# Performance work log

Hardware: AMD Instinct MI355X
Metric: run time of the kernel (lower is better)

Reference implementation:

```python
import jax, jax.numpy as jnp
import numpy as np

B, F, H, S, K, L, C = 128, 8192, 8192, 4, 32, 3, 100  # batch, encoded feats, hidden, segments, synapses/seg, hidden layers, classes


def setup_inputs() -> dict:
    key = jax.random.key(0)
    k1, k2, k3, k4, k5, k6 = jax.random.split(key, 6)
    # binary encoded input activations (thermometer-coded tabular features)
    x = jax.random.randint(k1, (B, F), 0, 2).astype(jnp.float32)
    # sign weights in {-1,+1} for each synapse of each segment of each neuron
    signs0 = jnp.where(jax.random.bernoulli(k2, 0.5, (S, H, K)), 1.0, -1.0).astype(jnp.float32)
    signsH = jnp.where(jax.random.bernoulli(k3, 0.5, (L - 1, S, H, K)), 1.0, -1.0).astype(jnp.float32)
    # synapse source indices (irregular connectivity)
    idx0 = jax.random.randint(k4, (S, H, K), 0, F, dtype=jnp.int32)
    idxH = jax.random.randint(k5, (L - 1, S, H, K), 0, H, dtype=jnp.int32)
    # per-layer output connection matrices [L, H, C]
    wout = jax.random.normal(k6, (L, H, C), dtype=jnp.float32) * 0.02
    return {"x": x, "signs0": signs0, "signsH": signsH, "wout": wout,
            "idx0": idx0, "idxH": idxH, "threshold": 8}


def _segment_layer(a, idx, signs, threshold):
    # a: [B, P] prev activations; idx/signs: [S, H, K]
    g = a[:, idx]                                  # [B, S, H, K] irregular gather
    z = jnp.einsum('bshk,shk->bsh', g, signs)      # per-segment summed input
    fired = jnp.any(z >= threshold, axis=1)        # OR over segments -> [B, H]
    return fired.astype(a.dtype)


def reference(x, signs0, signsH, wout, idx0, idxH, threshold):
    thr = jnp.float32(threshold)
    a = _segment_layer(x, idx0, signs0, thr)       # hidden layer 0
    acts = [a]
    for l in range(idxH.shape[0]):                 # remaining hidden layers (fixed small L)
        a = _segment_layer(a, idxH[l], signsH[l], thr)
        acts.append(a)
    # sum class votes from every hidden layer's output connection matrix
    out = jnp.einsum('lbh,lhc->bc', jnp.stack(acts, 0), wout)  # [B, C]
    return out
```

## Files before the change

### kernel.cpp

```cpp
#include <hip/hip_runtime.h>
#include <stdint.h>

#define B 128
#define F 8192
#define H 8192
#define S 4
#define K 32
#define L 3
#define C 100


__global__ void pack_x_kernel(const float* __restrict__ x, uint2* __restrict__ xPP,
                              float* __restrict__ out) {
    const int zi = blockIdx.x * 128 + threadIdx.x;
    if (zi < B * C) out[zi] = 0.0f;

    const int b  = threadIdx.x;
    const int wv = threadIdx.x >> 6;
    const int f0 = blockIdx.x * 32;
    const float4* xr = (const float4*)(x + (size_t)b * F + f0);
    for (int j = 0; j < 8; ++j) {
        const float4 v = xr[j];
        const uint64_t m0 = __ballot(v.x > 0.5f);
        const uint64_t m1 = __ballot(v.y > 0.5f);
        const uint64_t m2 = __ballot(v.z > 0.5f);
        const uint64_t m3 = __ballot(v.w > 0.5f);
        if ((threadIdx.x & 63) == 0) {
            const int f = f0 + 4 * j;
            uint4* dst = (uint4*)(xPP + (size_t)wv * F + f);
            dst[0] = make_uint4((uint32_t)m0, (uint32_t)(m0 >> 32),
                                (uint32_t)m1, (uint32_t)(m1 >> 32));
            dst[1] = make_uint4((uint32_t)m2, (uint32_t)(m2 >> 32),
                                (uint32_t)m3, (uint32_t)(m3 >> 32));
        }
    }
}

__device__ __forceinline__ int load_threshold(const int* p) {
    int v = *p;
    if (v >= (1 << 23)) v = (int)__int_as_float(v);
    return v;
}

__device__ __forceinline__ void cs5(uint32_t* a, uint32_t v) {
#pragma unroll
    for (int i = 0; i < 5; ++i) { const uint32_t t = a[i]; a[i] = t ^ v; v = t & v; }
}

__device__ __forceinline__ void pair_sum5(const uint32_t* x, uint32_t* y) {
    uint32_t c = 0;
#pragma unroll
    for (int i = 0; i < 5; ++i) {
        const uint32_t p = (uint32_t)__shfl_xor((int)x[i], 32);
        const uint32_t s = x[i] ^ p;
        y[i] = s ^ c;
        c = (x[i] & p) | (s & c);
    }
    y[5] = c;
}

__device__ __forceinline__ uint32_t fired_cmp(const uint32_t* A, const uint32_t* P, int thr) {
    uint32_t Y[7];
    uint32_t c = 0;
#pragma unroll
    for (int i = 0; i < 7; ++i) {
        const uint32_t ai = (i < 6) ? A[i] : 0u;
        const uint32_t bm = ((thr >> i) & 1) ? 0xFFFFFFFFu : 0u;
        const uint32_t t  = ai ^ bm;
        Y[i] = t ^ c;
        c = (ai & bm) | (t & c);
    }
    uint32_t bw = 0;
#pragma unroll
    for (int i = 0; i < 7; ++i) {
        const uint32_t xx = (i >= 1) ? P[i - 1] : 0u;
        const uint32_t d  = xx ^ Y[i];
        bw = ((~xx) & Y[i]) | ((~d) & bw);
    }
    return ~bw;
}

#define GLDS16(gp, lp)                                                \
    __builtin_amdgcn_global_load_lds(                                 \
        (const __attribute__((address_space(1))) uint32_t*)(gp),      \
        (__attribute__((address_space(3))) uint32_t*)(lp), 16, 0, 0)

#define HG 32
#define ISTRIDE 35

__global__ __launch_bounds__(512, 2) void layer_kernel(
        const uint32_t* __restrict__ prevPP,
        const int* __restrict__ idx,
        const float* __restrict__ signs,
        uint32_t* __restrict__ outPP,
        const int* __restrict__ thrp) {
    __shared__ uint2    tab[2 * H];
    __shared__ uint32_t isg[S * HG * ISTRIDE];
    __shared__ uint32_t fbuf[8 * HG * 2];

    const int tid = threadIdx.x;
    const int hg  = blockIdx.x;
    const int thr = load_threshold(thrp);

    {
        uint32_t* lbase = (uint32_t*)&tab[0];
#pragma unroll
        for (int i = 0; i < 16; ++i) {
            const int o = (i * 512 + tid) * 4;
            GLDS16(prevPP + o, lbase + o);
        }
    }
    {
        const int s    = tid >> 7;
        const int hrow = (tid & 127) >> 2;
        const int k0   = (tid & 3) * 8;
        const size_t gb = ((size_t)s * H + (size_t)hg * HG + hrow) * K + k0;
        const int4   ia = *(const int4*)(idx + gb);
        const int4   ic = *(const int4*)(idx + gb + 4);
        const float4 sa = *(const float4*)(signs + gb);
        const float4 sc = *(const float4*)(signs + gb + 4);
        uint32_t* dst = &isg[(s * HG + hrow) * ISTRIDE + k0];
        dst[0] = (uint32_t)ia.x | ((uint32_t)__float_as_int(sa.x) & 0x80000000u);
        dst[1] = (uint32_t)ia.y | ((uint32_t)__float_as_int(sa.y) & 0x80000000u);
        dst[2] = (uint32_t)ia.z | ((uint32_t)__float_as_int(sa.z) & 0x80000000u);
        dst[3] = (uint32_t)ia.w | ((uint32_t)__float_as_int(sa.w) & 0x80000000u);
        dst[4] = (uint32_t)ic.x | ((uint32_t)__float_as_int(sc.x) & 0x80000000u);
        dst[5] = (uint32_t)ic.y | ((uint32_t)__float_as_int(sc.y) & 0x80000000u);
        dst[6] = (uint32_t)ic.z | ((uint32_t)__float_as_int(sc.z) & 0x80000000u);
        dst[7] = (uint32_t)ic.w | ((uint32_t)__float_as_int(sc.w) & 0x80000000u);
    }
    __syncthreads();

    const int lane = tid & 63;
    const int ww   = tid >> 6;
    const int s    = ww & 3;
    const int wp   = ww >> 2;
    const int kh   = lane >> 5;
    const int h5   = lane & 31;

    uint32_t A0[5] = {0,0,0,0,0}, P0[5] = {0,0,0,0,0};
    uint32_t A1[5] = {0,0,0,0,0}, P1[5] = {0,0,0,0,0};
    const uint32_t* row = &isg[(s * HG + h5) * ISTRIDE + kh * 16];
    const uint2*    tw  = &tab[wp * H];
#pragma unroll
    for (int c8 = 0; c8 < 2; ++c8) {
        uint32_t iv[8];
#pragma unroll
        for (int j = 0; j < 8; ++j) iv[j] = row[c8 * 8 + j];
        uint2 g[8];
#pragma unroll
        for (int j = 0; j < 8; ++j) g[j] = tw[iv[j] & 0xFFFFu];
#pragma unroll
        for (int j = 0; j < 8; ++j) {
            const uint32_t pm = ~(uint32_t)((int32_t)iv[j] >> 31);
            cs5(A0, g[j].x);
            cs5(P0, g[j].x & pm);
            cs5(A1, g[j].y);
            cs5(P1, g[j].y & pm);
        }
    }

    uint32_t A0f[6], P0f[6], A1f[6], P1f[6];
    pair_sum5(A0, A0f);
    pair_sum5(P0, P0f);
    pair_sum5(A1, A1f);
    pair_sum5(P1, P1f);

    const uint32_t f0 = fired_cmp(A0f, P0f, thr);
    const uint32_t f1 = fired_cmp(A1f, P1f, thr);

    if (kh == 0) {
        fbuf[(ww * HG + h5) * 2 + 0] = f0;
        fbuf[(ww * HG + h5) * 2 + 1] = f1;
    }
    __syncthreads();

    if (tid < 128) {
        const int wp2  = tid >> 6;
        const int comp = (tid >> 5) & 1;
        const int hh   = tid & 31;
        uint32_t v = 0;
#pragma unroll
        for (int s2 = 0; s2 < 4; ++s2)
            v |= fbuf[((wp2 * 4 + s2) * HG + hh) * 2 + comp];
        outPP[((size_t)wp2 * H + (size_t)hg * HG + hh) * 2 + comp] = v;
    }
}

#define NHC 32
#define HCH (H / NHC)

__global__ void final_kernel(const uint32_t* __restrict__ actU,
                             const float* __restrict__ wout,
                             float* __restrict__ out) {
    const int lane = threadIdx.x & 63;
    const int wid  = threadIdx.x >> 6;
    const int hc   = blockIdx.x & (NHC - 1);
    const int bg   = blockIdx.x / NHC;
    const int b    = bg * 4 + wid;
    const int w32  = b >> 5;
    const int wp   = w32 >> 1;
    const int comp = w32 & 1;
    const int bit  = b & 31;

    float acc0 = 0.0f, acc1 = 0.0f;
    const int c1 = 64 + lane;
    const bool c1v = (c1 < C);

    for (int l = 0; l < L; ++l) {
        const uint32_t* aT = actU + ((size_t)(l * 2 + wp) * H) * 2 + comp;
        const float* wl = wout + (size_t)l * H * C;
        for (int r = 0; r < HCH / 64; ++r) {
            const int hbase = hc * HCH + r * 64;
            const uint32_t m = aT[(size_t)(hbase + lane) * 2];
            uint64_t hm = __ballot((m >> bit) & 1u);
            while (hm) {
                const int slot = __ffsll((unsigned long long)hm) - 1;
                hm &= hm - 1;
                const float* wr = wl + (size_t)(hbase + slot) * C;
                acc0 += wr[lane];
                if (c1v) acc1 += wr[c1];
            }
        }
    }
    atomicAdd(&out[b * C + lane], acc0);
    if (c1v) atomicAdd(&out[b * C + c1], acc1);
}

extern "C" void kernel_launch(void* const* d_in, const int* in_sizes, int n_in,
                              void* d_out, int out_size, void* d_ws, size_t ws_size,
                              hipStream_t stream) {
    const float* x      = (const float*)d_in[0];
    const float* signs0 = (const float*)d_in[1];
    const float* signsH = (const float*)d_in[2];
    const float* wout   = (const float*)d_in[3];
    const int*   idx0   = (const int*)d_in[4];
    const int*   idxH   = (const int*)d_in[5];
    const int*   thr    = (const int*)d_in[6];
    float* out = (float*)d_out;

    uint32_t* xPP   = (uint32_t*)d_ws;
    uint32_t* actPP = xPP + (size_t)4 * F;

    pack_x_kernel<<<F / 32, 128, 0, stream>>>(x, (uint2*)xPP, out);

    layer_kernel<<<H / HG, 512, 0, stream>>>(xPP, idx0, signs0, actPP, thr);
    layer_kernel<<<H / HG, 512, 0, stream>>>(actPP, idxH, signsH,
                                             actPP + (size_t)4 * H, thr);
    layer_kernel<<<H / HG, 512, 0, stream>>>(actPP + (size_t)4 * H,
                                             idxH + (size_t)S * H * K,
                                             signsH + (size_t)S * H * K,
                                             actPP + (size_t)8 * H, thr);

    final_kernel<<<32 * NHC, 256, 0, stream>>>(actPP, wout, out);
}
```

Before: 117.5 us.

## Fuse pack, three layers and readout into one cooperative kernel with grid syncs

Replaces the five separate launches (bit-pack, three layer kernels, final readout) with a single cooperative kernel of 256 blocks that uses grid-wide syncs between phases. The aim is to remove per-launch overhead and inter-kernel gaps, which matter because each phase is only tens of microseconds. In exchange it relies on all 256 blocks fitting co-resident, remaps the pack and final phases onto 512-thread blocks, and adds grid.sync costs. It falls back to the old multi-kernel path if the cooperative launch fails.

```diff
diff --git a/kernel.cpp b/kernel.cpp
--- a/kernel.cpp
+++ b/kernel.cpp
@@ -1,5 +1,8 @@
 #include <hip/hip_runtime.h>
+#include <hip/hip_cooperative_groups.h>
 #include <stdint.h>
+
+namespace cg = cooperative_groups;
 
 #define B 128
 #define F 8192
@@ -10,32 +13,6 @@
 #define C 100
 
 
-__global__ void pack_x_kernel(const float* __restrict__ x, uint2* __restrict__ xPP,
-                              float* __restrict__ out) {
-    const int zi = blockIdx.x * 128 + threadIdx.x;
-    if (zi < B * C) out[zi] = 0.0f;
-
-    const int b  = threadIdx.x;
-    const int wv = threadIdx.x >> 6;
-    const int f0 = blockIdx.x * 32;
-    const float4* xr = (const float4*)(x + (size_t)b * F + f0);
-    for (int j = 0; j < 8; ++j) {
-        const float4 v = xr[j];
-        const uint64_t m0 = __ballot(v.x > 0.5f);
-        const uint64_t m1 = __ballot(v.y > 0.5f);
-        const uint64_t m2 = __ballot(v.z > 0.5f);
-        const uint64_t m3 = __ballot(v.w > 0.5f);
-        if ((threadIdx.x & 63) == 0) {
-            const int f = f0 + 4 * j;
-            uint4* dst = (uint4*)(xPP + (size_t)wv * F + f);
-            dst[0] = make_uint4((uint32_t)m0, (uint32_t)(m0 >> 32),
-                                (uint32_t)m1, (uint32_t)(m1 >> 32));
-            dst[1] = make_uint4((uint32_t)m2, (uint32_t)(m2 >> 32),
-                                (uint32_t)m3, (uint32_t)(m3 >> 32));
-        }
-    }
-}
-
 __device__ __forceinline__ int load_threshold(const int* p) {
     int v = *p;
     if (v >= (1 << 23)) v = (int)__int_as_float(v);
@@ -88,22 +65,15 @@
 #define HG 32
 #define ISTRIDE 35
 
-__global__ __launch_bounds__(512, 2) void layer_kernel(
+__device__ __forceinline__ void layer_phase(
         const uint32_t* __restrict__ prevPP,
         const int* __restrict__ idx,
         const float* __restrict__ signs,
         uint32_t* __restrict__ outPP,
-        const int* __restrict__ thrp) {
-    __shared__ uint2    tab[2 * H];
-    __shared__ uint32_t isg[S * HG * ISTRIDE];
-    __shared__ uint32_t fbuf[8 * HG * 2];
-
-    const int tid = threadIdx.x;
-    const int hg  = blockIdx.x;
-    const int thr = load_threshold(thrp);
-
+        const int thr, const int hg, const int tid,
+        uint2* tab, uint32_t* isg, uint32_t* fbuf) {
     {
-        uint32_t* lbase = (uint32_t*)&tab[0];
+        uint32_t* lbase = (uint32_t*)tab;
 #pragma unroll
         for (int i = 0; i < 16; ++i) {
             const int o = (i * 512 + tid) * 4;
@@ -187,6 +157,140 @@
     }
 }
 
+__global__ __launch_bounds__(512, 2) void fused_kernel(
+        const float* __restrict__ x,
+        const int* __restrict__ idx0, const float* __restrict__ signs0,
+        const int* __restrict__ idxH, const float* __restrict__ signsH,
+        const float* __restrict__ wout, const int* __restrict__ thrp,
+        uint2* __restrict__ xPP, uint32_t* __restrict__ actPP,
+        float* __restrict__ out) {
+    __shared__ uint2    tab[2 * H];
+    __shared__ uint32_t isg[S * HG * ISTRIDE];
+    __shared__ uint32_t fbuf[8 * HG * 2];
+
+    cg::grid_group grid = cg::this_grid();
+    const int tid = threadIdx.x;
+    const int bid = blockIdx.x;
+    const int thr = load_threshold(thrp);
+
+    {
+        const int zi = bid * 512 + tid;
+        if (zi < B * C) out[zi] = 0.0f;
+
+        const int b   = tid & 127;
+        const int wv  = (tid >> 6) & 1;
+        const int sub = tid >> 7;
+        const int f0  = bid * 32;
+        const float4* xr = (const float4*)(x + (size_t)b * F + f0);
+#pragma unroll
+        for (int jj = 0; jj < 2; ++jj) {
+            const int j = sub * 2 + jj;
+            const float4 v = xr[j];
+            const uint64_t m0 = __ballot(v.x > 0.5f);
+            const uint64_t m1 = __ballot(v.y > 0.5f);
+            const uint64_t m2 = __ballot(v.z > 0.5f);
+            const uint64_t m3 = __ballot(v.w > 0.5f);
+            if ((tid & 63) == 0) {
+                const int f = f0 + 4 * j;
+                uint4* dst = (uint4*)(xPP + (size_t)wv * F + f);
+                dst[0] = make_uint4((uint32_t)m0, (uint32_t)(m0 >> 32),
+                                    (uint32_t)m1, (uint32_t)(m1 >> 32));
+                dst[1] = make_uint4((uint32_t)m2, (uint32_t)(m2 >> 32),
+                                    (uint32_t)m3, (uint32_t)(m3 >> 32));
+            }
+        }
+    }
+    __threadfence();
+    grid.sync();
+
+    layer_phase((const uint32_t*)xPP, idx0, signs0, actPP,
+                thr, bid, tid, tab, isg, fbuf);
+    __threadfence();
+    grid.sync();
+
+    layer_phase(actPP, idxH, signsH, actPP + (size_t)4 * H,
+                thr, bid, tid, tab, isg, fbuf);
+    __threadfence();
+    grid.sync();
+
+    layer_phase(actPP + (size_t)4 * H, idxH + (size_t)S * H * K,
+                signsH + (size_t)S * H * K, actPP + (size_t)8 * H,
+                thr, bid, tid, tab, isg, fbuf);
+    __threadfence();
+    grid.sync();
+
+    {
+        const int lane = tid & 63;
+        const int gw   = bid * 8 + (tid >> 6);
+        const int b    = gw >> 4;
+        const int hc   = gw & 15;
+        const int w32  = b >> 5;
+        const int wp   = w32 >> 1;
+        const int comp = w32 & 1;
+        const int bit  = b & 31;
+
+        float acc0 = 0.0f, acc1 = 0.0f;
+        const int c1 = 64 + lane;
+        const bool c1v = (c1 < C);
+
+        for (int l = 0; l < L; ++l) {
+            const uint32_t* aT = actPP + ((size_t)(l * 2 + wp) * H) * 2 + comp;
+            const float* wl = wout + (size_t)l * H * C;
+            for (int r = 0; r < 8; ++r) {
+                const int hbase = hc * 512 + r * 64;
+                const uint32_t m = aT[(size_t)(hbase + lane) * 2];
+                uint64_t hm = __ballot((m >> bit) & 1u);
+                while (hm) {
+                    const int slot = __ffsll((unsigned long long)hm) - 1;
+                    hm &= hm - 1;
+                    const float* wr = wl + (size_t)(hbase + slot) * C;
+                    acc0 += wr[lane];
+                    if (c1v) acc1 += wr[c1];
+                }
+            }
+        }
+        atomicAdd(&out[b * C + lane], acc0);
+        if (c1v) atomicAdd(&out[b * C + c1], acc1);
+    }
+}
+
+__global__ void pack_x_kernel(const float* __restrict__ x, uint2* __restrict__ xPP,
+                              float* __restrict__ out) {
+    const int zi = blockIdx.x * 128 + threadIdx.x;
+    if (zi < B * C) out[zi] = 0.0f;
+
+    const int b  = threadIdx.x;
+    const int wv = threadIdx.x >> 6;
+    const int f0 = blockIdx.x * 32;
+    const float4* xr = (const float4*)(x + (size_t)b * F + f0);
+    for (int j = 0; j < 8; ++j) {
+        const float4 v = xr[j];
+        const uint64_t m0 = __ballot(v.x > 0.5f);
+        const uint64_t m1 = __ballot(v.y > 0.5f);
+        const uint64_t m2 = __ballot(v.z > 0.5f);
+        const uint64_t m3 = __ballot(v.w > 0.5f);
+        if ((threadIdx.x & 63) == 0) {
+            const int f = f0 + 4 * j;
+            uint4* dst = (uint4*)(xPP + (size_t)wv * F + f);
+            dst[0] = make_uint4((uint32_t)m0, (uint32_t)(m0 >> 32),
+                                (uint32_t)m1, (uint32_t)(m1 >> 32));
+            dst[1] = make_uint4((uint32_t)m2, (uint32_t)(m2 >> 32),
+                                (uint32_t)m3, (uint32_t)(m3 >> 32));
+        }
+    }
+}
+
+__global__ __launch_bounds__(512, 2) void layer_kernel(
+        const uint32_t* __restrict__ prevPP, const int* __restrict__ idx,
+        const float* __restrict__ signs, uint32_t* __restrict__ outPP,
+        const int* __restrict__ thrp) {
+    __shared__ uint2    tab[2 * H];
+    __shared__ uint32_t isg[S * HG * ISTRIDE];
+    __shared__ uint32_t fbuf[8 * HG * 2];
+    layer_phase(prevPP, idx, signs, outPP, load_threshold(thrp),
+                blockIdx.x, threadIdx.x, tab, isg, fbuf);
+}
+
 #define NHC 32
 #define HCH (H / NHC)
 
@@ -241,16 +345,24 @@
 
     uint32_t* xPP   = (uint32_t*)d_ws;
     uint32_t* actPP = xPP + (size_t)4 * F;
-
-    pack_x_kernel<<<F / 32, 128, 0, stream>>>(x, (uint2*)xPP, out);
-
-    layer_kernel<<<H / HG, 512, 0, stream>>>(xPP, idx0, signs0, actPP, thr);
-    layer_kernel<<<H / HG, 512, 0, stream>>>(actPP, idxH, signsH,
-                                             actPP + (size_t)4 * H, thr);
-    layer_kernel<<<H / HG, 512, 0, stream>>>(actPP + (size_t)4 * H,
-                                             idxH + (size_t)S * H * K,
-                                             signsH + (size_t)S * H * K,
-                                             actPP + (size_t)8 * H, thr);
-
-    final_kernel<<<32 * NHC, 256, 0, stream>>>(actPP, wout, out);
-}
+    uint2*    xPP2  = (uint2*)d_ws;
+
+    void* args[] = { (void*)&x, (void*)&idx0, (void*)&signs0,
+                     (void*)&idxH, (void*)&signsH, (void*)&wout, (void*)&thr,
+                     (void*)&xPP2, (void*)&actPP, (void*)&out };
+    hipError_t e = hipLaunchCooperativeKernel((const void*)fused_kernel,
+                                              dim3(256), dim3(512),
+                                              args, 0, stream);
+    if (e != hipSuccess) {
+        (void)hipGetLastError();
+        pack_x_kernel<<<F / 32, 128, 0, stream>>>(x, xPP2, out);
+        layer_kernel<<<H / HG, 512, 0, stream>>>(xPP, idx0, signs0, actPP, thr);
+        layer_kernel<<<H / HG, 512, 0, stream>>>(actPP, idxH, signsH,
+                                                 actPP + (size_t)4 * H, thr);
+        layer_kernel<<<H / HG, 512, 0, stream>>>(actPP + (size_t)4 * H,
+                                                 idxH + (size_t)S * H * K,
+                                                 signsH + (size_t)S * H * K,
+                                                 actPP + (size_t)8 * H, thr);
+        final_kernel<<<32 * NHC, 256, 0, stream>>>(actPP, wout, out);
+    }
+}
```

Result: slower. 374.0 us (+218.3%).

## Fuse three layer kernels and final vote into one persistent kernel with grid barriers

Applied to the files above, without the earlier changes.

Replaces the three per-layer launches and the final vote kernel with one persistent kernel of 256 blocks. The batch is split into two 64-row halves, each handled by its own block group, so every block keeps only its half's activation table in LDS. Layers are separated by a software grid barrier per half, built from atomic counters that the pack kernel zeroes. The goal is to remove launch gaps and shrink LDS use to raise occupancy, at the cost of a spin barrier that assumes all blocks are co-resident and breaks out after a bounded wait.

```diff
diff --git a/kernel.cpp b/kernel.cpp
--- a/kernel.cpp
+++ b/kernel.cpp
@@ -9,11 +9,187 @@
 #define L 3
 #define C 100
 
-
-__global__ void pack_x_kernel(const float* __restrict__ x, uint2* __restrict__ xPP,
-                              float* __restrict__ out) {
+#define NBLK 256
+#define NTHR 512
+
+
+__device__ __forceinline__ int load_threshold(const int* p) {
+    int v = *p;
+    if (v >= (1 << 23)) v = (int)__int_as_float(v);
+    return v;
+}
+
+__device__ __forceinline__ void cs5(uint32_t* a, uint32_t v) {
+#pragma unroll
+    for (int i = 0; i < 5; ++i) { const uint32_t t = a[i]; a[i] = t ^ v; v = t & v; }
+}
+
+__device__ __forceinline__ void pair_sum5(const uint32_t* x, uint32_t* y) {
+    uint32_t c = 0;
+#pragma unroll
+    for (int i = 0; i < 5; ++i) {
+        const uint32_t p = (uint32_t)__shfl_xor((int)x[i], 32);
+        const uint32_t s = x[i] ^ p;
+        y[i] = s ^ c;
+        c = (x[i] & p) | (s & c);
+    }
+    y[5] = c;
+}
+
+__device__ __forceinline__ uint32_t fired_cmp(const uint32_t* A, const uint32_t* P, int thr) {
+    uint32_t Y[7];
+    uint32_t c = 0;
+#pragma unroll
+    for (int i = 0; i < 7; ++i) {
+        const uint32_t ai = (i < 6) ? A[i] : 0u;
+        const uint32_t bm = ((thr >> i) & 1) ? 0xFFFFFFFFu : 0u;
+        const uint32_t t  = ai ^ bm;
+        Y[i] = t ^ c;
+        c = (ai & bm) | (t & c);
+    }
+    uint32_t bw = 0;
+#pragma unroll
+    for (int i = 0; i < 7; ++i) {
+        const uint32_t xx = (i >= 1) ? P[i - 1] : 0u;
+        const uint32_t d  = xx ^ Y[i];
+        bw = ((~xx) & Y[i]) | ((~d) & bw);
+    }
+    return ~bw;
+}
+
+#define GLDS16(gp, lp)                                                \
+    __builtin_amdgcn_global_load_lds(                                 \
+        (const __attribute__((address_space(1))) uint32_t*)(gp),      \
+        (__attribute__((address_space(3))) uint32_t*)(lp), 16, 0, 0)
+
+#define AG_LOAD(p)                                                          \
+    __hip_atomic_load((p), __ATOMIC_RELAXED, __HIP_MEMORY_SCOPE_AGENT)
+#define AG_STORE(p, v)                                                      \
+    __hip_atomic_store((p), (v), __ATOMIC_RELAXED, __HIP_MEMORY_SCOPE_AGENT)
+
+__device__ __forceinline__ void wp_barrier(uint32_t* wbar, uint32_t ep,
+                                           int tid, int gidx) {
+    asm volatile("s_waitcnt vmcnt(0)" ::: "memory");
+    __syncthreads();
+    if (tid == 0) {
+        const uint32_t t = __hip_atomic_fetch_add(&wbar[gidx * 16], 1u,
+                               __ATOMIC_RELAXED, __HIP_MEMORY_SCOPE_AGENT) + 1u;
+        if (t == ep * 16u) {
+            const uint32_t r = __hip_atomic_fetch_add(&wbar[128], 1u,
+                               __ATOMIC_RELAXED, __HIP_MEMORY_SCOPE_AGENT) + 1u;
+            if (r == ep * 8u) AG_STORE(&wbar[160], ep);
+        }
+        int guard = 0;
+        while (AG_LOAD(&wbar[160]) < ep) {
+            __builtin_amdgcn_s_sleep(2);
+            if (++guard > (1 << 17)) break;
+        }
+    }
+    __syncthreads();
+    asm volatile("" ::: "memory");
+}
+
+__device__ __forceinline__ void layer_phase(
+        const uint32_t* __restrict__ prevPlane,
+        const int* __restrict__ idx,
+        const float* __restrict__ signs,
+        uint32_t* __restrict__ outPlane,
+        const int thr, const int hg, const int tid,
+        uint2* tab, uint32_t* fbuf) {
+    const int lane = tid & 63;
+    const int ww   = tid >> 6;
+    const int s    = ww & 3;
+    const int rh   = ww >> 2;
+    const int kh   = lane >> 5;
+    const int h5   = lane & 31;
+    const int hloc = rh * 32 + h5;
+    const int h    = hg * 64 + hloc;
+
+    const size_t gb = ((size_t)s * H + h) * K + kh * 16;
+    const int4   i0 = *(const int4*)(idx + gb);
+    const int4   i1 = *(const int4*)(idx + gb + 4);
+    const int4   i2 = *(const int4*)(idx + gb + 8);
+    const int4   i3 = *(const int4*)(idx + gb + 12);
+    const float4 s0 = *(const float4*)(signs + gb);
+    const float4 s1 = *(const float4*)(signs + gb + 4);
+    const float4 s2 = *(const float4*)(signs + gb + 8);
+    const float4 s3 = *(const float4*)(signs + gb + 12);
+
+    {
+        uint32_t* lbase = (uint32_t*)tab;
+#pragma unroll
+        for (int i = 0; i < 8; ++i) {
+            const int o = (i * 512 + tid) * 4;
+            GLDS16(prevPlane + o, lbase + o);
+        }
+    }
+    __syncthreads();
+
+    const uint32_t iv[16] = {
+        (uint32_t)i0.x, (uint32_t)i0.y, (uint32_t)i0.z, (uint32_t)i0.w,
+        (uint32_t)i1.x, (uint32_t)i1.y, (uint32_t)i1.z, (uint32_t)i1.w,
+        (uint32_t)i2.x, (uint32_t)i2.y, (uint32_t)i2.z, (uint32_t)i2.w,
+        (uint32_t)i3.x, (uint32_t)i3.y, (uint32_t)i3.z, (uint32_t)i3.w };
+    const uint32_t pm[16] = {
+        ~(uint32_t)(__float_as_int(s0.x) >> 31), ~(uint32_t)(__float_as_int(s0.y) >> 31),
+        ~(uint32_t)(__float_as_int(s0.z) >> 31), ~(uint32_t)(__float_as_int(s0.w) >> 31),
+        ~(uint32_t)(__float_as_int(s1.x) >> 31), ~(uint32_t)(__float_as_int(s1.y) >> 31),
+        ~(uint32_t)(__float_as_int(s1.z) >> 31), ~(uint32_t)(__float_as_int(s1.w) >> 31),
+        ~(uint32_t)(__float_as_int(s2.x) >> 31), ~(uint32_t)(__float_as_int(s2.y) >> 31),
+        ~(uint32_t)(__float_as_int(s2.z) >> 31), ~(uint32_t)(__float_as_int(s2.w) >> 31),
+        ~(uint32_t)(__float_as_int(s3.x) >> 31), ~(uint32_t)(__float_as_int(s3.y) >> 31),
+        ~(uint32_t)(__float_as_int(s3.z) >> 31), ~(uint32_t)(__float_as_int(s3.w) >> 31) };
+
+    uint32_t A0[5] = {0,0,0,0,0}, P0[5] = {0,0,0,0,0};
+    uint32_t A1[5] = {0,0,0,0,0}, P1[5] = {0,0,0,0,0};
+#pragma unroll
+    for (int c8 = 0; c8 < 2; ++c8) {
+        uint2 g[8];
+#pragma unroll
+        for (int j = 0; j < 8; ++j) g[j] = tab[iv[c8 * 8 + j]];
+#pragma unroll
+        for (int j = 0; j < 8; ++j) {
+            const uint32_t pmv = pm[c8 * 8 + j];
+            cs5(A0, g[j].x);
+            cs5(P0, g[j].x & pmv);
+            cs5(A1, g[j].y);
+            cs5(P1, g[j].y & pmv);
+        }
+    }
+
+    uint32_t A0f[6], P0f[6], A1f[6], P1f[6];
+    pair_sum5(A0, A0f);
+    pair_sum5(P0, P0f);
+    pair_sum5(A1, A1f);
+    pair_sum5(P1, P1f);
+
+    const uint32_t f0 = fired_cmp(A0f, P0f, thr);
+    const uint32_t f1 = fired_cmp(A1f, P1f, thr);
+
+    if (kh == 0) {
+        fbuf[((s * 2 + rh) * 32 + h5) * 2 + 0] = f0;
+        fbuf[((s * 2 + rh) * 32 + h5) * 2 + 1] = f1;
+    }
+    __syncthreads();
+
+    if (tid < 128) {
+        const int rr   = tid >> 6;
+        const int hh   = (tid >> 1) & 31;
+        const int comp = tid & 1;
+        uint32_t v = 0;
+#pragma unroll
+        for (int s2 = 0; s2 < 4; ++s2)
+            v |= fbuf[((s2 * 2 + rr) * 32 + hh) * 2 + comp];
+        AG_STORE(&outPlane[(size_t)(hg * 64 + rr * 32 + hh) * 2 + comp], v);
+    }
+}
+
+__global__ __launch_bounds__(128) void init_pack_kernel(
+        const float* __restrict__ x, uint2* __restrict__ xPP,
+        float* __restrict__ out, uint32_t* __restrict__ bar) {
     const int zi = blockIdx.x * 128 + threadIdx.x;
     if (zi < B * C) out[zi] = 0.0f;
+    if (blockIdx.x < 4) bar[blockIdx.x * 128 + threadIdx.x] = 0u;
 
     const int b  = threadIdx.x;
     const int wv = threadIdx.x >> 6;
@@ -36,195 +212,86 @@
     }
 }
 
-__device__ __forceinline__ int load_threshold(const int* p) {
-    int v = *p;
-    if (v >= (1 << 23)) v = (int)__int_as_float(v);
-    return v;
-}
-
-__device__ __forceinline__ void cs5(uint32_t* a, uint32_t v) {
-#pragma unroll
-    for (int i = 0; i < 5; ++i) { const uint32_t t = a[i]; a[i] = t ^ v; v = t & v; }
-}
-
-__device__ __forceinline__ void pair_sum5(const uint32_t* x, uint32_t* y) {
-    uint32_t c = 0;
-#pragma unroll
-    for (int i = 0; i < 5; ++i) {
-        const uint32_t p = (uint32_t)__shfl_xor((int)x[i], 32);
-        const uint32_t s = x[i] ^ p;
-        y[i] = s ^ c;
-        c = (x[i] & p) | (s & c);
-    }
-    y[5] = c;
-}
-
-__device__ __forceinline__ uint32_t fired_cmp(const uint32_t* A, const uint32_t* P, int thr) {
-    uint32_t Y[7];
-    uint32_t c = 0;
-#pragma unroll
-    for (int i = 0; i < 7; ++i) {
-        const uint32_t ai = (i < 6) ? A[i] : 0u;
-        const uint32_t bm = ((thr >> i) & 1) ? 0xFFFFFFFFu : 0u;
-        const uint32_t t  = ai ^ bm;
-        Y[i] = t ^ c;
-        c = (ai & bm) | (t & c);
-    }
-    uint32_t bw = 0;
-#pragma unroll
-    for (int i = 0; i < 7; ++i) {
-        const uint32_t xx = (i >= 1) ? P[i - 1] : 0u;
-        const uint32_t d  = xx ^ Y[i];
-        bw = ((~xx) & Y[i]) | ((~d) & bw);
-    }
-    return ~bw;
-}
-
-#define GLDS16(gp, lp)                                                \
-    __builtin_amdgcn_global_load_lds(                                 \
-        (const __attribute__((address_space(1))) uint32_t*)(gp),      \
-        (__attribute__((address_space(3))) uint32_t*)(lp), 16, 0, 0)
-
-#define HG 32
-#define ISTRIDE 35
-
-__global__ __launch_bounds__(512, 2) void layer_kernel(
-        const uint32_t* __restrict__ prevPP,
-        const int* __restrict__ idx,
-        const float* __restrict__ signs,
-        uint32_t* __restrict__ outPP,
-        const int* __restrict__ thrp) {
-    __shared__ uint2    tab[2 * H];
-    __shared__ uint32_t isg[S * HG * ISTRIDE];
-    __shared__ uint32_t fbuf[8 * HG * 2];
+__global__ __launch_bounds__(512, 4) void fused_kernel(
+        const uint32_t* __restrict__ xPP,
+        const int* __restrict__ idx0, const float* __restrict__ signs0,
+        const int* __restrict__ idxH, const float* __restrict__ signsH,
+        const float* __restrict__ wout, const int* __restrict__ thrp,
+        uint32_t* __restrict__ actPP, float* __restrict__ out,
+        uint32_t* __restrict__ bar) {
+    __shared__ uint2    tab[H];
+    __shared__ uint32_t fbuf[4 * 2 * 32 * 2];
 
     const int tid = threadIdx.x;
-    const int hg  = blockIdx.x;
+    const int bid = blockIdx.x;
+    const int wp  = bid & 1;
+    const int hg  = bid >> 1;
     const int thr = load_threshold(thrp);
 
+    uint32_t* wbar = bar + wp * 256;
+    const int gidx = (bid >> 1) & 7;
+
+    const uint32_t* xPlane = xPP + (size_t)wp * 2 * F;
+    uint32_t* pl0 = actPP + (size_t)(0 * 2 + wp) * 2 * H;
+    uint32_t* pl1 = actPP + (size_t)(1 * 2 + wp) * 2 * H;
+    uint32_t* pl2 = actPP + (size_t)(2 * 2 + wp) * 2 * H;
+
+    const int*   idx2   = idxH;
+    const float* signs2 = signsH;
+    const int*   idx3   = idxH + (size_t)S * H * K;
+    const float* signs3 = signsH + (size_t)S * H * K;
+
+    layer_phase(xPlane, idx0, signs0, pl0, thr, hg, tid, tab, fbuf);
+    wp_barrier(wbar, 1, tid, gidx);
+
+    layer_phase(pl0, idx2, signs2, pl1, thr, hg, tid, tab, fbuf);
+    wp_barrier(wbar, 2, tid, gidx);
+
+    layer_phase(pl1, idx3, signs3, pl2, thr, hg, tid, tab, fbuf);
+    wp_barrier(wbar, 3, tid, gidx);
+
     {
-        uint32_t* lbase = (uint32_t*)&tab[0];
-#pragma unroll
-        for (int i = 0; i < 16; ++i) {
-            const int o = (i * 512 + tid) * 4;
-            GLDS16(prevPP + o, lbase + o);
-        }
-    }
-    {
-        const int s    = tid >> 7;
-        const int hrow = (tid & 127) >> 2;
-        const int k0   = (tid & 3) * 8;
-        const size_t gb = ((size_t)s * H + (size_t)hg * HG + hrow) * K + k0;
-        const int4   ia = *(const int4*)(idx + gb);
-        const int4   ic = *(const int4*)(idx + gb + 4);
-        const float4 sa = *(const float4*)(signs + gb);
-        const float4 sc = *(const float4*)(signs + gb + 4);
-        uint32_t* dst = &isg[(s * HG + hrow) * ISTRIDE + k0];
-        dst[0] = (uint32_t)ia.x | ((uint32_t)__float_as_int(sa.x) & 0x80000000u);
-        dst[1] = (uint32_t)ia.y | ((uint32_t)__float_as_int(sa.y) & 0x80000000u);
-        dst[2] = (uint32_t)ia.z | ((uint32_t)__float_as_int(sa.z) & 0x80000000u);
-        dst[3] = (uint32_t)ia.w | ((uint32_t)__float_as_int(sa.w) & 0x80000000u);
-        dst[4] = (uint32_t)ic.x | ((uint32_t)__float_as_int(sc.x) & 0x80000000u);
-        dst[5] = (uint32_t)ic.y | ((uint32_t)__float_as_int(sc.y) & 0x80000000u);
-        dst[6] = (uint32_t)ic.z | ((uint32_t)__float_as_int(sc.z) & 0x80000000u);
-        dst[7] = (uint32_t)ic.w | ((uint32_t)__float_as_int(sc.w) & 0x80000000u);
-    }
-    __syncthreads();
-
-    const int lane = tid & 63;
-    const int ww   = tid >> 6;
-    const int s    = ww & 3;
-    const int wp   = ww >> 2;
-    const int kh   = lane >> 5;
-    const int h5   = lane & 31;
-
-    uint32_t A0[5] = {0,0,0,0,0}, P0[5] = {0,0,0,0,0};
-    uint32_t A1[5] = {0,0,0,0,0}, P1[5] = {0,0,0,0,0};
-    const uint32_t* row = &isg[(s * HG + h5) * ISTRIDE + kh * 16];
-    const uint2*    tw  = &tab[wp * H];
-#pragma unroll
-    for (int c8 = 0; c8 < 2; ++c8) {
-        uint32_t iv[8];
-#pragma unroll
-        for (int j = 0; j < 8; ++j) iv[j] = row[c8 * 8 + j];
-        uint2 g[8];
-#pragma unroll
-        for (int j = 0; j < 8; ++j) g[j] = tw[iv[j] & 0xFFFFu];
-#pragma unroll
-        for (int j = 0; j < 8; ++j) {
-            const uint32_t pm = ~(uint32_t)((int32_t)iv[j] >> 31);
-            cs5(A0, g[j].x);
-            cs5(P0, g[j].x & pm);
-            cs5(A1, g[j].y);
-            cs5(P1, g[j].y & pm);
-        }
-    }
-
-    uint32_t A0f[6], P0f[6], A1f[6], P1f[6];
-    pair_sum5(A0, A0f);
-    pair_sum5(P0, P0f);
-    pair_sum5(A1, A1f);
-    pair_sum5(P1, P1f);
-
-    const uint32_t f0 = fired_cmp(A0f, P0f, thr);
-    const uint32_t f1 = fired_cmp(A1f, P1f, thr);
-
-    if (kh == 0) {
-        fbuf[(ww * HG + h5) * 2 + 0] = f0;
-        fbuf[(ww * HG + h5) * 2 + 1] = f1;
-    }
-    __syncthreads();
-
-    if (tid < 128) {
-        const int wp2  = tid >> 6;
-        const int comp = (tid >> 5) & 1;
-        const int hh   = tid & 31;
-        uint32_t v = 0;
-#pragma unroll
-        for (int s2 = 0; s2 < 4; ++s2)
-            v |= fbuf[((wp2 * 4 + s2) * HG + hh) * 2 + comp];
-        outPP[((size_t)wp2 * H + (size_t)hg * HG + hh) * 2 + comp] = v;
-    }
-}
-
-#define NHC 32
-#define HCH (H / NHC)
-
-__global__ void final_kernel(const uint32_t* __restrict__ actU,
-                             const float* __restrict__ wout,
-                             float* __restrict__ out) {
-    const int lane = threadIdx.x & 63;
-    const int wid  = threadIdx.x >> 6;
-    const int hc   = blockIdx.x & (NHC - 1);
-    const int bg   = blockIdx.x / NHC;
-    const int b    = bg * 4 + wid;
-    const int w32  = b >> 5;
-    const int wp   = w32 >> 1;
-    const int comp = w32 & 1;
-    const int bit  = b & 31;
-
-    float acc0 = 0.0f, acc1 = 0.0f;
-    const int c1 = 64 + lane;
-    const bool c1v = (c1 < C);
-
-    for (int l = 0; l < L; ++l) {
-        const uint32_t* aT = actU + ((size_t)(l * 2 + wp) * H) * 2 + comp;
-        const float* wl = wout + (size_t)l * H * C;
-        for (int r = 0; r < HCH / 64; ++r) {
-            const int hbase = hc * HCH + r * 64;
-            const uint32_t m = aT[(size_t)(hbase + lane) * 2];
-            uint64_t hm = __ballot((m >> bit) & 1u);
-            while (hm) {
-                const int slot = __ffsll((unsigned long long)hm) - 1;
-                hm &= hm - 1;
-                const float* wr = wl + (size_t)(hbase + slot) * C;
-                acc0 += wr[lane];
-                if (c1v) acc1 += wr[c1];
+        const int lane = tid & 63;
+        const int gw   = bid * 8 + (tid >> 6);
+        const int b    = gw >> 4;
+        const int hc   = gw & 15;
+        const int w32  = b >> 5;
+        const int fwp  = w32 >> 1;
+        const int comp = w32 & 1;
+        const int bit  = b & 31;
+
+        uint32_t mv[L][8];
+#pragma unroll
+        for (int l = 0; l < L; ++l) {
+            const uint32_t* aT = actPP + (size_t)(l * 2 + fwp) * 2 * H + comp;
+#pragma unroll
+            for (int r = 0; r < 8; ++r)
+                mv[l][r] = AG_LOAD(&aT[(size_t)(hc * 512 + r * 64 + lane) * 2]);
+        }
+
+        float acc0 = 0.0f, acc1 = 0.0f;
+        const int c1 = 64 + lane;
+        const bool c1v = (c1 < C);
+
+#pragma unroll
+        for (int l = 0; l < L; ++l) {
+            const float* wl = wout + (size_t)l * H * C;
+#pragma unroll
+            for (int r = 0; r < 8; ++r) {
+                const int hbase = hc * 512 + r * 64;
+                uint64_t hm = __ballot((mv[l][r] >> bit) & 1u);
+                while (hm) {
+                    const int slot = __ffsll((unsigned long long)hm) - 1;
+                    hm &= hm - 1;
+                    const float* wr = wl + (size_t)(hbase + slot) * C;
+                    acc0 += wr[lane];
+                    if (c1v) acc1 += wr[c1];
+                }
             }
         }
-    }
-    atomicAdd(&out[b * C + lane], acc0);
-    if (c1v) atomicAdd(&out[b * C + c1], acc1);
+        atomicAdd(&out[b * C + lane], acc0);
+        if (c1v) atomicAdd(&out[b * C + c1], acc1);
+    }
 }
 
 extern "C" void kernel_launch(void* const* d_in, const int* in_sizes, int n_in,
@@ -241,16 +308,10 @@
 
     uint32_t* xPP   = (uint32_t*)d_ws;
     uint32_t* actPP = xPP + (size_t)4 * F;
-
-    pack_x_kernel<<<F / 32, 128, 0, stream>>>(x, (uint2*)xPP, out);
-
-    layer_kernel<<<H / HG, 512, 0, stream>>>(xPP, idx0, signs0, actPP, thr);
-    layer_kernel<<<H / HG, 512, 0, stream>>>(actPP, idxH, signsH,
-                                             actPP + (size_t)4 * H, thr);
-    layer_kernel<<<H / HG, 512, 0, stream>>>(actPP + (size_t)4 * H,
-                                             idxH + (size_t)S * H * K,
-                                             signsH + (size_t)S * H * K,
-                                             actPP + (size_t)8 * H, thr);
-
-    final_kernel<<<32 * NHC, 256, 0, stream>>>(actPP, wout, out);
-}
+    uint32_t* bar   = actPP + (size_t)12 * H;
+    uint2*    xPP2  = (uint2*)d_ws;
+
+    init_pack_kernel<<<F / 32, 128, 0, stream>>>(x, xPP2, out, bar);
+    fused_kernel<<<NBLK, NTHR, 0, stream>>>(xPP, idx0, signs0, idxH, signsH,
+                                            wout, thr, actPP, out, bar);
+}
```

Measured after the change: 129.2 us. 1.1x slower.
